# Kernel optimization log

Hardware: AMD Instinct MI355X
Metric: run time of the kernel (lower is better)

## Reference

```python
import jax, jax.numpy as jnp
import numpy as np

B = 2048; IN_DIM = 60; TTL = 30; H = 512; L = 5; OUT = 23
T_PTS = 90; SUB = 10  # fixed-step RK4 substeps per day (stands in for per-sample dopri5)
P_D = 0.2; P_H = 0.15; P_V = 0.25  # DELPHI fixed detection/hospitalization/ventilation fractions
LN2 = float(np.log(2.0))
R_I = LN2/5.0; R_D = LN2/2.0; R_RI = LN2/10.0; R_RH = LN2/15.0; R_RV = LN2/10.0


def setup_inputs():
    ks = jax.random.split(jax.random.key(0), 24)
    w = lambda k, s: (jax.random.normal(k, s) * 0.05).astype(jnp.float32)
    rng = jnp.array([1.0]*11 + [1.0, 60.0, 4.0, 0.5, 0.3, 0.5, 5.0, 5.0, 2.0, 60.0, 30.0, 1.0], dtype=jnp.float32)
    return {
        'model_input': jax.random.normal(ks[0], (B, IN_DIM), dtype=jnp.float32),
        'population': jax.random.uniform(ks[1], (B,), minval=1e5, maxval=1e7, dtype=jnp.float32),
        'cumulative_case_number': jax.random.uniform(ks[2], (B, 1), minval=1e3, maxval=1e5, dtype=jnp.float32),
        'mortality_rate': jax.random.uniform(ks[3], (B,), minval=0.01, maxval=0.05, dtype=jnp.float32),
        'h0': jax.random.normal(ks[4], (L, B, H), dtype=jnp.float32),
        'c0': jax.random.normal(ks[5], (L, B, H), dtype=jnp.float32),
        'W_ih0': w(ks[6], (4*H, TTL)),
        'W_ihR': w(ks[7], (L-1, 4*H, H)),
        'W_hh': w(ks[8], (L, 4*H, H)),
        'b_ih': w(ks[9], (L, 4*H)),
        'b_hh': w(ks[10], (L, 4*H)),
        'meta_W1': w(ks[11], (H, IN_DIM - TTL)), 'meta_b1': w(ks[12], (H,)),
        'meta_W2': w(ks[13], (H, H)), 'meta_b2': w(ks[14], (H,)),
        'ro_W1': w(ks[15], (2*H, 2*H)), 'ro_b1': w(ks[16], (2*H,)),
        'ro_W2': w(ks[17], (OUT, 2*H)), 'ro_b2': w(ks[18], (OUT,)),
        'dnn_output_range': rng,
        'sigmoid_scale': 1,
    }


def _backbone(model_input, population, h0, c0, W_ih0, W_ihR, W_hh, b_ih, b_hh,
              meta_W1, meta_b1, meta_W2, meta_b2, ro_W1, ro_b1, ro_W2, ro_b2,
              dnn_output_range, sigmoid_scale):
    x = model_input[:, :TTL] / population[:, None]
    for l in range(L):  # single-timestep, 5-layer LSTM; torch gate order i,f,g,o
        Wi = W_ih0 if l == 0 else W_ihR[l-1]
        g = x @ Wi.T + b_ih[l] + h0[l] @ W_hh[l].T + b_hh[l]
        gi, gf, gg, go = jnp.split(g, 4, axis=1)
        c = jax.nn.sigmoid(gf) * c0[l] + jax.nn.sigmoid(gi) * jnp.tanh(gg)
        x = jax.nn.sigmoid(go) * jnp.tanh(c)
    ts_out = x  # [B, H]
    m = jax.nn.relu(model_input[:, TTL:] @ meta_W1.T + meta_b1)
    m = jax.nn.relu(m @ meta_W2.T + meta_b2)
    z = jnp.concatenate([ts_out, m], axis=1)  # [B, 2H]
    z = jnp.tanh(z @ ro_W1.T + ro_b1)
    raw = z @ ro_W2.T + ro_b2  # [B, OUT]
    dnn = jax.nn.sigmoid(raw * sigmoid_scale) * dnn_output_range
    return dnn, ts_out, raw


def _ode(dnn, population, cumulative_case_number, mortality_rate):
    p = dnn[:, 11:]  # 12 fitted DELPHI params per sample
    alpha, days, r_s, r_dth, p_dth, r_dthdecay, k1, k2, jump, t_jump, std_normal, k3 = [p[:, j] for j in range(12)]
    N = population
    PopI = cumulative_case_number[:, 0]
    PopD = jnp.floor(mortality_rate * PopI)
    R_0 = jnp.where(PopI - PopD > 5.0 * PopD, 5.0 * PopD, 0.0)
    PopCI = PopI - PopD - R_0
    # DELPHI initial conditions
    S0 = N - (PopCI/P_D)*(k1 + k2) - R_0/P_D - PopD/P_D
    y0 = jnp.stack([
        S0,
        PopCI/P_D*k1,                      # E
        PopCI/P_D*k2,                      # I
        (PopCI/P_D - PopCI)*(1.0 - p_dth), # AR
        PopCI*P_H*(1.0 - p_dth),           # DHR
        PopCI*(1.0 - P_H)*(1.0 - p_dth),   # DQR
        (PopCI/P_D - PopCI)*p_dth,         # AD
        PopCI*P_H*p_dth,                   # DHD
        PopCI*(1.0 - P_H)*p_dth,           # DQD
        R_0/P_D,                           # R
        PopD/P_D,                          # D
        PopCI*P_H,                         # TH
        PopCI*P_H*P_V*(1.0 - p_dth),       # DVR
        PopCI*P_H*P_V*p_dth,               # DVD
        PopD,                              # DD
        PopI,                              # DT
    ], axis=1)  # [B, 16]

    def deriv(t, y):
        S, E, I = y[:, 0], y[:, 1], y[:, 2]
        AR, DHR, DQR, AD, DHD, DQD = y[:, 3], y[:, 4], y[:, 5], y[:, 6], y[:, 7], y[:, 8]
        DVR, DVD = y[:, 12], y[:, 13]
        gam = (2.0/jnp.pi)*jnp.arctan(-(t - days)/20.0*r_s) + 1.0 \
              + jump*jnp.exp(-(t - t_jump)**2/(2.0*std_normal**2))
        pdt = (2.0/jnp.pi)*(p_dth - 0.001)*(jnp.arctan(-t*r_dthdecay/20.0) + jnp.pi/2.0) + 0.001
        inf = alpha*gam*S*I/N
        det = R_D*I
        return jnp.stack([
            -inf,
            inf - R_I*E,
            R_I*E - det,
            det*(1.0-pdt)*(1.0-P_D) - R_RI*AR,
            det*(1.0-pdt)*P_D*P_H - R_RH*DHR,
            det*(1.0-pdt)*P_D*(1.0-P_H) - R_RI*DQR,
            det*pdt*(1.0-P_D) - r_dth*AD,
            det*pdt*P_D*P_H - r_dth*DHD,
            det*pdt*P_D*(1.0-P_H) - r_dth*DQD,
            R_RI*(AR + DQR) + R_RH*DHR,
            r_dth*(AD + DQD + DHD),
            det*P_D*P_H,
            det*(1.0-pdt)*P_D*P_H*P_V - R_RV*DVR,
            det*pdt*P_D*P_H*P_V - r_dth*DVD,
            r_dth*(DHD + DQD),
            det*P_D,
        ], axis=1)

    dt = 1.0 / SUB

    def segment(y, t0):
        def sub(yy, j):
            t = t0 + j*dt
            k1_ = deriv(t, yy)
            k2_ = deriv(t + 0.5*dt, yy + 0.5*dt*k1_)
            k3_ = deriv(t + 0.5*dt, yy + 0.5*dt*k2_)
            k4_ = deriv(t + dt, yy + dt*k3_)
            return yy + (dt/6.0)*(k1_ + 2.0*k2_ + 2.0*k3_ + k4_), None
        y2, _ = jax.lax.scan(sub, y, jnp.arange(SUB, dtype=jnp.float32))
        return y2, y2

    _, ys = jax.lax.scan(segment, y0, jnp.arange(T_PTS - 1, dtype=jnp.float32))
    sol = jnp.concatenate([y0[None], ys], axis=0)  # [T_PTS, B, 16]
    return jnp.transpose(sol, (1, 0, 2))  # [B, T_PTS, 16]


def reference(model_input, population, cumulative_case_number, mortality_rate, h0, c0,
              W_ih0, W_ihR, W_hh, b_ih, b_hh, meta_W1, meta_b1, meta_W2, meta_b2,
              ro_W1, ro_b1, ro_W2, ro_b2, dnn_output_range, sigmoid_scale):
    dnn, ts_out, raw = _backbone(model_input, population, h0, c0, W_ih0, W_ihR, W_hh,
                                 b_ih, b_hh, meta_W1, meta_b1, meta_W2, meta_b2,
                                 ro_W1, ro_b1, ro_W2, ro_b2, dnn_output_range, sigmoid_scale)
    sol = _ode(dnn, population, cumulative_case_number, mortality_rate)
    return sol, dnn, ts_out[:, None, :], raw
```

## Files before the change

kernel.cpp:

```cpp
#include <hip/hip_runtime.h>
#include <hip/hip_bf16.h>
#include <math.h>

#define BATCH 2048
#define HID 512
#define TPTS 90
#define NSEG 89
#define NSUB 10
#define NSTEPS 890

__device__ __constant__ const float kR_I  = 0.6931471805599453f / 5.0f;
__device__ __constant__ const float kR_D  = 0.6931471805599453f / 2.0f;
__device__ __constant__ const float kR_RI = 0.6931471805599453f / 10.0f;
__device__ __constant__ const float kR_RH = 0.6931471805599453f / 15.0f;
__device__ __constant__ const float kR_RV = 0.6931471805599453f / 10.0f;

typedef __attribute__((ext_vector_type(8))) short short8;
typedef __attribute__((ext_vector_type(4))) short short4v;
typedef __attribute__((ext_vector_type(4))) float float4v;

__device__ __forceinline__ float sigmoidf_(float x) { return 1.0f / (1.0f + expf(-x)); }

__global__ void prep_pad(const float* __restrict__ mi, const float* __restrict__ pop,
                         const float* __restrict__ Wih0, const float* __restrict__ mW1,
// ... 3 lines not shown
    int i = blockIdx.x * 256 + threadIdx.x;
    int r = i >> 5, c = i & 31;
    bool v = (c < 30);
    x0p[i] = v ? mi[r * 60 + c] / pop[r] : 0.0f;
    xmp[i] = v ? mi[r * 60 + 30 + c] : 0.0f;
    Wp0[i] = v ? Wih0[r * 30 + c] : 0.0f;
    if (r < 512) Wpm[i] = v ? mW1[r * 30 + c] : 0.0f;
}

__device__ __forceinline__ void pack_quad(const float* __restrict__ s1, int ld1, int K1,
                                          const float* __restrict__ s2, int ld2, int K2,
                                          __hip_bfloat16* __restrict__ dst, int idx, bool wm)
{
    int Ks = K1 + K2, Kq = Ks >> 2;
    int r = idx / Kq, k4 = (idx - r * Kq) << 2;
    const float* srcp; int base, seg, kk;
    if (k4 < K1) { srcp = s1 + (size_t)r * ld1 + k4; base = 0; seg = K1; kk = k4; }
    else { kk = k4 - K1; srcp = s2 + (size_t)r * ld2 + kk; base = 3 * K1; seg = K2; }
    float4 x = *(const float4*)srcp;
    union { __hip_bfloat16 b[4]; short4v v; } H, L;
    H.b[0] = __float2bfloat16(x.x); H.b[1] = __float2bfloat16(x.y);
    H.b[2] = __float2bfloat16(x.z); H.b[3] = __float2bfloat16(x.w);
    L.b[0] = __float2bfloat16(x.x - __bfloat162float(H.b[0]));
    L.b[1] = __float2bfloat16(x.y - __bfloat162float(H.b[1]));
    L.b[2] = __float2bfloat16(x.z - __bfloat162float(H.b[2]));
    L.b[3] = __float2bfloat16(x.w - __bfloat162float(H.b[3]));
    __hip_bfloat16* d = dst + (size_t)r * (3 * Ks) + base;
    *(short4v*)(d + kk)           = H.v;
    *(short4v*)(d + seg + kk)     = wm ? L.v : H.v;
    *(short4v*)(d + 2 * seg + kk) = wm ? H.v : L.v;
}

__global__ void pack_pair(const float* __restrict__ a1, int alda1, int aK1,
                          const float* __restrict__ a2, int alda2, int aK2,
                          __hip_bfloat16* __restrict__ da, int arows,
                          const float* __restrict__ w1, int wld1, int wK1,
                          const float* __restrict__ w2, int wld2, int wK2,
                          __hip_bfloat16* __restrict__ dw, int wrows)
{
    int aKq = (aK1 + aK2) >> 2, wKq = (wK1 + wK2) >> 2;
    int qa = arows * aKq;
    int idx = blockIdx.x * 256 + threadIdx.x;
    if (idx < qa) {
        pack_quad(a1, alda1, aK1, a2, alda2, aK2, da, idx, false);
    } else {
        idx -= qa;
        if (idx < wrows * wKq) pack_quad(w1, wld1, wK1, w2, wld2, wK2, dw, idx, true);
    }
}

template<int ACT>
__global__ __launch_bounds__(256, 2)
void gemm_mfma(const __hip_bfloat16* __restrict__ Ah,
               const __hip_bfloat16* __restrict__ Wh, int K3, int kHalf,
               const float* __restrict__ b1, const float* __restrict__ b2,
               float* __restrict__ Cp, float* __restrict__ Cp2, int ldc, int N)
{
    __shared__ __hip_bfloat16 As[128 * 32];
    __shared__ __hip_bfloat16 Ws[128 * 32];
    const int tid  = threadIdx.x;
    const int m0   = blockIdx.y * 128;
    const int n0   = blockIdx.x * 128;
    const int z    = blockIdx.z;
    const int k0   = z ? kHalf : 0;
    const int kLen = (kHalf == 0) ? K3 : (z ? (K3 - kHalf) : kHalf);
    float* C = z ? Cp2 : Cp;
    const int lane = tid & 63, wv = tid >> 6;
    const int mw   = (wv >> 1) * 64, nw = (wv & 1) * 64;
    const int l15  = lane & 15, quad = lane >> 4;
    const int sr   = tid >> 2;
    const int sc   = (tid & 3) * 8;

    float4v acc[4][4];
    #pragma unroll
    for (int i = 0; i < 4; ++i)
        #pragma unroll
        for (int j = 0; j < 4; ++j)
            acc[i][j] = (float4v){0.0f, 0.0f, 0.0f, 0.0f};

    const __hip_bfloat16* pa0 = Ah + (size_t)(m0 + sr)      * K3 + k0 + sc;
    const __hip_bfloat16* pa1 = Ah + (size_t)(m0 + sr + 64) * K3 + k0 + sc;
    const __hip_bfloat16* pw0 = Wh + (size_t)(n0 + sr)      * K3 + k0 + sc;
    const __hip_bfloat16* pw1 = Wh + (size_t)(n0 + sr + 64) * K3 + k0 + sc;

    short8 a0 = *(const short8*)(pa0);
    short8 a1 = *(const short8*)(pa1);
    short8 w0 = *(const short8*)(pw0);
    short8 w1 = *(const short8*)(pw1);

    for (int kt = 0; kt < kLen; kt += 32) {
        __syncthreads();
        *(short8*)(As + sr * 32 + sc)        = a0;
        *(short8*)(As + (sr + 64) * 32 + sc) = a1;
        *(short8*)(Ws + sr * 32 + sc)        = w0;
        *(short8*)(Ws + (sr + 64) * 32 + sc) = w1;
        __syncthreads();

        int kn = kt + 32;
        if (kn < kLen) {
            a0 = *(const short8*)(pa0 + kn);
            a1 = *(const short8*)(pa1 + kn);
            w0 = *(const short8*)(pw0 + kn);
            w1 = *(const short8*)(pw1 + kn);
        }

        short8 af[4], bf[4];
        #pragma unroll
        for (int t = 0; t < 4; ++t) {
            af[t] = *(const short8*)(As + (mw + t * 16 + l15) * 32 + quad * 8);
            bf[t] = *(const short8*)(Ws + (nw + t * 16 + l15) * 32 + quad * 8);
        }
        #pragma unroll
        for (int i = 0; i < 4; ++i)
            #pragma unroll
            for (int j = 0; j < 4; ++j)
                acc[i][j] = __builtin_amdgcn_mfma_f32_16x16x32_bf16(af[i], bf[j], acc[i][j], 0, 0, 0);
    }

    #pragma unroll
    for (int j = 0; j < 4; ++j) {
        int col = n0 + nw + j * 16 + l15;
        float bias = z ? 0.0f : (b1[col] + (b2 ? b2[col] : 0.0f));
        #pragma unroll
        for (int i = 0; i < 4; ++i) {
            #pragma unroll
            for (int r = 0; r < 4; ++r) {
                int row = m0 + mw + i * 16 + quad * 4 + r;
                float v = acc[i][j][r] + bias;
                if (ACT == 1)      v = fmaxf(v, 0.0f);
                else if (ACT == 2) v = tanhf(v);
                C[(size_t)row * ldc + col] = v;
            }
        }
    }
}

template<int ACT>
__global__ __launch_bounds__(256)
void gemm_dual(const float* __restrict__ A1, int lda1,
               const float* __restrict__ W1, int ldw1, int K1,
               const float* __restrict__ A2, int lda2,
               const float* __restrict__ W2, int ldw2, int K2,
               const float* __restrict__ b1p, const float* __restrict__ b2p,
               float* __restrict__ Cp, int ldc, int N)
{
    __shared__ float As[8][128];
    __shared__ float Ws[8][128];
    const int tid  = threadIdx.x;
    const int m0   = blockIdx.y * 128;
    const int n0   = blockIdx.x * 128;
    const int tm   = tid >> 4;
    const int tn   = tid & 15;
    const int lrow = tid >> 1;
    const int lkh  = (tid & 1) << 2;
    const int wrow = n0 + lrow;
    const int Ktot = K1 + K2;

    float acc[8][8];
    #pragma unroll
    for (int i = 0; i < 8; ++i)
        #pragma unroll
        for (int j = 0; j < 8; ++j) acc[i][j] = 0.0f;

    float4 av = *(const float4*)(A1 + (size_t)(m0 + lrow) * lda1 + lkh);
    float4 wv = make_float4(0.0f, 0.0f, 0.0f, 0.0f);
    if (wrow < N) wv = *(const float4*)(W1 + (size_t)wrow * ldw1 + lkh);

    for (int kt = 0; kt < Ktot; kt += 8) {
        __syncthreads();
        As[lkh + 0][lrow] = av.x; As[lkh + 1][lrow] = av.y;
        As[lkh + 2][lrow] = av.z; As[lkh + 3][lrow] = av.w;
        Ws[lkh + 0][lrow] = wv.x; Ws[lkh + 1][lrow] = wv.y;
        Ws[lkh + 2][lrow] = wv.z; Ws[lkh + 3][lrow] = wv.w;
        __syncthreads();

// ... 109 lines not shown
        const float* g2 = G1 + (size_t)m * 2048 + h;
        gi += g2[0]; gf += g2[512]; gg += g2[1024]; go += g2[1536];
    }
    float c = sigmoidf_(gf) * c0l[i] + sigmoidf_(gi) * tanhf(gg);
    float x = sigmoidf_(go) * tanhf(c);
    xout[(size_t)m * xld + h] = x;
    if (ts) ts[i] = x;
}

__global__ void dnn_kernel(const float* __restrict__ raw, const int* __restrict__ ssp,
                           const float* __restrict__ rng, float* __restrict__ dnn)
{
    int i = blockIdx.x * 256 + threadIdx.x;
    if (i >= 2048 * 23) return;
    int c = i % 23;
    int v = *ssp;
    float ss = (v > 100000 || v < 0) ? __int_as_float(v) : (float)v;
    dnn[i] = sigmoidf_(raw[i] * ss) * rng[c];
}

__device__ __forceinline__ void gampdt_eval(float t, float alpha, float days, float rs20,
                                            float jump, float t_jump, float inv2s2,
                                            float pconst, float rdd20, float* ag, float* pd)
{
    float dtj = t - t_jump;
    float g = 0.6366197723675814f * atanf((days - t) * rs20) + 1.0f + jump * expf(-(dtj * dtj) * inv2s2);
    *ag = alpha * g;
    *pd = pconst * (atanf(-t * rdd20) + 1.5707963267948966f) + 0.001f;
}

__global__ void gampdt4_kernel(const float* __restrict__ dnn, const float* __restrict__ pop,
                               float4* __restrict__ ag4)
{
    int idx = blockIdx.x * 256 + threadIdx.x;
    if (idx >= NSTEPS * 2048) return;
    int e = idx & 2047;
    int k = idx >> 11;
    int s = k / 10, j = k - s * 10;
    const float* p = dnn + e * 23 + 11;
    float alpha = p[0], days = p[1], r_s = p[2], p_dth = p[4], r_dthdecay = p[5];
    float jump = p[8], t_jump = p[9], stdn = p[10];
    float invN = 1.0f / pop[e];
    float rs20   = r_s * 0.05f;
    float rdd20  = r_dthdecay * 0.05f;
    float inv2s2 = 1.0f / (2.0f * stdn * stdn);
    float pconst = 0.6366197723675814f * (p_dth - 0.001f);
    float t = (float)s + (float)j * 0.1f;
    float agh, pdh, ag1, pd1;
    gampdt_eval(t + 0.05f, alpha, days, rs20, jump, t_jump, inv2s2, pconst, rdd20, &agh, &pdh);
    gampdt_eval(t + 0.1f,  alpha, days, rs20, jump, t_jump, inv2s2, pconst, rdd20, &ag1, &pd1);
    ag4[idx] = make_float4(agh * invN, pdh, ag1 * invN, pd1);
}

__global__ __launch_bounds__(64)
void ode_core(const float* __restrict__ dnn, const float* __restrict__ pop,
              const float* __restrict__ ccn, const float* __restrict__ mort,
              const float4* __restrict__ ag4, float4* __restrict__ det4,
              float* __restrict__ sol)
{
    int e = blockIdx.x * 64 + threadIdx.x;
    const float* p = dnn + e * 23 + 11;
    float alpha = p[0], days = p[1], r_s = p[2], k1p = p[6], k2p = p[7];
    float jump = p[8], t_jump = p[9], stdn = p[10], p_dth = p[4], rdd = p[5];

    float N = pop[e];
    float invN = 1.0f / N;
    float PopI = ccn[e];
    float PopD = floorf(mort[e] * PopI);
    float R0v  = (PopI - PopD > 5.0f * PopD) ? 5.0f * PopD : 0.0f;
    float PopCI = PopI - PopD - R0v;
    float DP = PopCI / 0.2f;

    float y0 = N - DP * (k1p + k2p) - R0v / 0.2f - PopD / 0.2f;
    float y1 = DP * k1p;
    float y2 = DP * k2p;
    float y11 = PopCI * 0.15f;
    float y15 = PopI;

    float* sole = sol + (size_t)e * (TPTS * 16);
    sole[0] = y0; sole[1] = y1; sole[2] = y2; sole[11] = y11; sole[15] = y15;

    float rs20   = r_s * 0.05f;
    float rdd20  = rdd * 0.05f;
    float inv2s2 = 1.0f / (2.0f * stdn * stdn);
    float pconst = 0.6366197723675814f * (p_dth - 0.001f);
    float ag0, pd0;
    gampdt_eval(0.0f, alpha, days, rs20, jump, t_jump, inv2s2, pconst, rdd20, &ag0, &pd0);
    float agI = ag0 * invN;

    float4 cv[10];
    #pragma unroll
    for (int j = 0; j < 10; ++j) cv[j] = ag4[(size_t)j * 2048 + e];

    const float h6 = 0.016666668f;
    for (int s = 0; s < NSEG; ++s) {
        float Sdet = 0.0f;
        float4 db[10];
        #pragma unroll
        for (int j = 0; j < 10; ++j) {
            float agh = cv[j].x, ag1 = cv[j].z;
            int kn = (s + 1) * 10 + j;
            if (kn >= NSTEPS) kn = NSTEPS - 1;
            cv[j] = ag4[(size_t)kn * 2048 + e];

            float det1 = kR_D * y2;
            float t1   = kR_I * y1;
            float inf  = agI * y0 * y2;
            float d1 = inf - t1, d2 = t1 - det1;
            float a0 = -inf, a1 = d1, a2 = d2;
            float z0 = y0 - 0.05f * inf, z1 = y1 + 0.05f * d1, z2 = y2 + 0.05f * d2;
            float det2 = kR_D * z2; t1 = kR_I * z1; inf = agh * z0 * z2;
            d1 = inf - t1; d2 = t1 - det2;
            a0 -= 2.0f * inf; a1 += 2.0f * d1; a2 += 2.0f * d2;
            z0 = y0 - 0.05f * inf; z1 = y1 + 0.05f * d1; z2 = y2 + 0.05f * d2;
            float det3 = kR_D * z2; t1 = kR_I * z1; inf = agh * z0 * z2;
            d1 = inf - t1; d2 = t1 - det3;
            a0 -= 2.0f * inf; a1 += 2.0f * d1; a2 += 2.0f * d2;
            z0 = y0 - 0.1f * inf; z1 = y1 + 0.1f * d1; z2 = y2 + 0.1f * d2;
            float det4v = kR_D * z2; t1 = kR_I * z1; inf = ag1 * z0 * z2;
            d1 = inf - t1; d2 = t1 - det4v;
            a0 -= inf; a1 += d1; a2 += d2;

            y0 += h6 * a0; y1 += h6 * a1; y2 += h6 * a2;
            float Wd = det1;
            Wd += 2.0f * det2; Wd += 2.0f * det3; Wd += det4v;
            Sdet += Wd;
            db[j] = make_float4(det1, det2, det3, det4v);
            agI = ag1;
        }
        #pragma unroll
        for (int j = 0; j < 10; ++j)
            det4[(size_t)(s * 10 + j) * 2048 + e] = db[j];
        y11 += h6 * (0.03f * Sdet);
        y15 += h6 * (0.2f * Sdet);
        float* sp = sole + (size_t)(s + 1) * 16;
        sp[0] = y0; sp[1] = y1; sp[2] = y2; sp[11] = y11; sp[15] = y15;
    }
}

__global__ __launch_bounds__(64)
void ode_decay(const float* __restrict__ dnn, const float* __restrict__ ccn,
               const float* __restrict__ mort, const float4* __restrict__ ag4,
               const float4* __restrict__ det4, float* __restrict__ sol)
{
    const int t  = blockIdx.x * 64 + threadIdx.x;
    const int e  = t >> 3;
    const int g  = t & 7;
    const int lane = threadIdx.x & 63;
    const int base = lane & ~7;

    const float* p = dnn + e * 23 + 11;
    float r_dth = p[3], p_dth = p[4];

    float PopI = ccn[e];
    float PopD = floorf(mort[e] * PopI);
    float R0v  = (PopI - PopD > 5.0f * PopD) ? 5.0f * PopD : 0.0f;
    float PopCI = PopI - PopD - R0v;
    float DP = PopCI / 0.2f;
    float ompd = 1.0f - p_dth;

    float iy3  = (DP - PopCI) * ompd;
    float iy4  = PopCI * 0.15f * ompd;
    float iy5  = PopCI * 0.85f * ompd;
    float iy6  = (DP - PopCI) * p_dth;
    float iy7  = PopCI * 0.15f * p_dth;
    float iy8  = PopCI * 0.85f * p_dth;
    float iy12 = PopCI * 0.15f * 0.25f * ompd;
    float iy13 = PopCI * 0.15f * 0.25f * p_dth;

    float ha = (g == 0) ? iy3 : (g == 1) ? iy4 : (g == 2) ? iy5 : iy6;
    float hb = (g == 4) ? iy7 : (g == 5) ? iy8 : (g == 6) ? iy12 : iy13;
    float ys = (g < 4) ? ha : hb;
    float c1 = (g == 0) ? 0.8f : (g == 1) ? 0.03f : (g == 2) ? 0.17f : (g == 6) ? 0.0075f : 0.0f;
    float c2 = (g == 3) ? 0.8f : (g == 4) ? 0.03f : (g == 5) ? 0.17f : (g == 7) ? 0.0075f : 0.0f;
    float rr = (g == 0 || g == 2) ? kR_RI : (g == 1) ? kR_RH : (g == 6) ? kR_RV : r_dth;
    int own_idx = (g < 4) ? ((g < 2) ? (g == 0 ? 3 : 4) : (g == 2 ? 5 : 6))
                          : ((g < 6) ? (g == 4 ? 7 : 8) : (g == 6 ? 12 : 13));

    float y9  = R0v / 0.2f;
    float y10 = PopD / 0.2f;
    float y14 = PopD;

    float* sole = sol + (size_t)e * (TPTS * 16);
    sole[own_idx] = ys;
    if (g == 0) sole[9]  = y9;
    if (g == 1) sole[10] = y10;
    if (g == 2) sole[14] = y14;

    float pconst = 0.6366197723675814f * (p_dth - 0.001f);
    float pd0 = pconst * 1.5707963267948966f + 0.001f;
    float u0 = c1 * (1.0f - pd0) + c2 * pd0;

    float4 cvd[10], cva[10];
    #pragma unroll
    for (int j = 0; j < 10; ++j) {
        cvd[j] = det4[(size_t)j * 2048 + e];
        cva[j] = ag4[(size_t)j * 2048 + e];
    }

    const float h6 = 0.016666668f;
    for (int s = 0; s < NSEG; ++s) {
        float Sy = 0.0f;
        #pragma unroll
        for (int j = 0; j < 10; ++j) {
            float4 dd = cvd[j];
            float pdh = cva[j].y, pd1 = cva[j].w;
            int kn = (s + 1) * 10 + j;
            if (kn >= NSTEPS) kn = NSTEPS - 1;
            cvd[j] = det4[(size_t)kn * 2048 + e];
            cva[j] = ag4[(size_t)kn * 2048 + e];

            float uh = c1 * (1.0f - pdh) + c2 * pdh;
            float u1 = c1 * (1.0f - pd1) + c2 * pd1;
            float k1v = dd.x * u0 - rr * ys;
            float zs1 = ys + 0.05f * k1v;
            float k2v = dd.y * uh - rr * zs1;
            float zs2 = ys + 0.05f * k2v;
            float k3v = dd.z * uh - rr * zs2;
            float zs3 = ys + 0.1f * k3v;
            float k4v = dd.w * u1 - rr * zs3;
            float ka = k1v + 2.0f * (k2v + k3v) + k4v;
            Sy += ys + 2.0f * (zs1 + zs2) + zs3;
            ys += h6 * ka;
            u0 = u1;
        }
        float S0 = __shfl(Sy, base + 0, 64);
        float S1 = __shfl(Sy, base + 1, 64);
        float S2 = __shfl(Sy, base + 2, 64);
        float S3 = __shfl(Sy, base + 3, 64);
        float S4 = __shfl(Sy, base + 4, 64);
        float S5 = __shfl(Sy, base + 5, 64);
        y9  += h6 * (kR_RI * (S0 + S2) + kR_RH * S1);
        y10 += h6 * (r_dth * ((S3 + S4) + S5));
        y14 += h6 * (r_dth * (S4 + S5));

        float* sp = sole + (size_t)(s + 1) * 16;
        sp[own_idx] = ys;
        if (g == 0) sp[9]  = y9;
        if (g == 1) sp[10] = y10;
        if (g == 2) sp[14] = y14;
    }
}

__device__ __forceinline__ void deriv16(const float* y, float ag, float pd,
                                        float invN, float r_dth, float* d)
{
    float inf = ag * y[0] * y[2] * invN;
    float det = kR_D * y[2];
    float t1  = kR_I * y[1];
    float omp = 1.0f - pd;
    float dq  = det * omp;
    float dp  = det * pd;
    float dq003 = dq * 0.03f;
    float dp003 = dp * 0.03f;
    d[0]  = -inf;
    d[1]  = inf - t1;
    d[2]  = t1 - det;
    d[3]  = dq * 0.8f  - kR_RI * y[3];
    d[4]  = dq003      - kR_RH * y[4];
    d[5]  = dq * 0.17f - kR_RI * y[5];
    d[6]  = dp * 0.8f  - r_dth * y[6];
    d[7]  = dp003      - r_dth * y[7];
    d[8]  = dp * 0.17f - r_dth * y[8];
    d[9]  = kR_RI * (y[3] + y[5]) + kR_RH * y[4];
    d[10] = r_dth * ((y[6] + y[7]) + y[8]);
    d[11] = det * 0.03f;
    d[12] = 0.25f * dq003 - kR_RV * y[12];
    d[13] = 0.25f * dp003 - r_dth * y[13];
    d[14] = r_dth * (y[7] + y[8]);
    d[15] = det * 0.2f;
}

__global__ __launch_bounds__(64)
void ode_kernel(const float* __restrict__ dnn, const float* __restrict__ pop,
                const float* __restrict__ ccn, const float* __restrict__ mort,
                float* __restrict__ sol)
{
    int e = blockIdx.x * 64 + threadIdx.x;
    const float* p = dnn + e * 23 + 11;
    float alpha = p[0], days = p[1], r_s = p[2], r_dth = p[3], p_dth = p[4];
    float r_dthdecay = p[5], k1p = p[6], k2p = p[7], jump = p[8], t_jump = p[9], stdn = p[10];

    float N = pop[e];
    float invN = 1.0f / N;
    float PopI = ccn[e];
    float PopD = floorf(mort[e] * PopI);
    float R0v  = (PopI - PopD > 5.0f * PopD) ? 5.0f * PopD : 0.0f;
    float PopCI = PopI - PopD - R0v;
    float DP = PopCI / 0.2f;

    float y[16];
    y[0]  = N - DP * (k1p + k2p) - R0v / 0.2f - PopD / 0.2f;
    y[1]  = DP * k1p;
    y[2]  = DP * k2p;
    y[3]  = (DP - PopCI) * (1.0f - p_dth);
    y[4]  = PopCI * 0.15f * (1.0f - p_dth);
    y[5]  = PopCI * 0.85f * (1.0f - p_dth);
    y[6]  = (DP - PopCI) * p_dth;
    y[7]  = PopCI * 0.15f * p_dth;
    y[8]  = PopCI * 0.85f * p_dth;
    y[9]  = R0v / 0.2f;
    y[10] = PopD / 0.2f;
    y[11] = PopCI * 0.15f;
    y[12] = PopCI * 0.15f * 0.25f * (1.0f - p_dth);
    y[13] = PopCI * 0.15f * 0.25f * p_dth;
    y[14] = PopD;
    y[15] = PopI;

    {
        float* sp = sol + (size_t)e * (TPTS * 16);
        #pragma unroll
        for (int i = 0; i < 16; ++i) sp[i] = y[i];
    }

    float rs20   = r_s * 0.05f;
    float rdd20  = r_dthdecay * 0.05f;
    float inv2s2 = 1.0f / (2.0f * stdn * stdn);
    float pconst = 0.6366197723675814f * (p_dth - 0.001f);

    float ag0, pd0;
    gampdt_eval(0.0f, alpha, days, rs20, jump, t_jump, inv2s2, pconst, rdd20, &ag0, &pd0);

    for (int s = 0; s < NSEG; ++s) {
        float t0 = (float)s;
        for (int j = 0; j < NSUB; ++j) {
            float agh, pdh, ag1, pd1;
// ... 15 lines not shown
            for (int i = 0; i < 16; ++i) y[i] += 0.016666668f * (acc[i] + d[i]);
            ag0 = ag1; pd0 = pd1;
        }
        float* sp = sol + (size_t)e * (TPTS * 16) + (size_t)(s + 1) * 16;
        #pragma unroll
        for (int i = 0; i < 16; ++i) sp[i] = y[i];
    }
}

extern "C" void kernel_launch(void* const* d_in, const int* in_sizes, int n_in,
                              void* d_out, int out_size, void* d_ws, size_t ws_size,
                              hipStream_t stream)
{
    const float* mi   = (const float*)d_in[0];
    const float* pop  = (const float*)d_in[1];
    const float* ccn  = (const float*)d_in[2];
    const float* mort = (const float*)d_in[3];
    const float* h0   = (const float*)d_in[4];
    const float* c0   = (const float*)d_in[5];
    const float* Wih0 = (const float*)d_in[6];
    const float* WihR = (const float*)d_in[7];
    const float* Whh  = (const float*)d_in[8];
    const float* bih  = (const float*)d_in[9];
    const float* bhh  = (const float*)d_in[10];
    const float* mW1  = (const float*)d_in[11];
    const float* mb1  = (const float*)d_in[12];
    const float* mW2  = (const float*)d_in[13];
    const float* mb2  = (const float*)d_in[14];
    const float* rW1  = (const float*)d_in[15];
    const float* rb1  = (const float*)d_in[16];
    const float* rW2  = (const float*)d_in[17];
    const float* rb2  = (const float*)d_in[18];
    const float* rng  = (const float*)d_in[19];
    const int*   ssp  = (const int*)d_in[20];

    float* out   = (float*)d_out;
    float* sol_o = out;
    float* dnn_o = out + 2949120;
    float* ts_o  = out + 2949120 + 47104;
    float* raw_o = out + 2949120 + 47104 + 1048576;

    float* ws  = (float*)d_ws;
    float* G   = ws;
    float* Z   = ws + 4194304;
    float* X0  = ws + 6291456;
    float* X1  = ws + 7340032;
    float* x0p = ws + 8388608;
    float* xmp = ws + 8454144;
    float* Wp0 = ws + 8519680;
    float* Wpm = ws + 8585216;
    __hip_bfloat16* Ab = (__hip_bfloat16*)(ws + 8601600);
    __hip_bfloat16* Wb = (__hip_bfloat16*)(ws + 8601600 + 3145728);
    float4* AG4  = (float4*)(ws + 8601600);
    float4* DET4 = (float4*)ws;
    float*  G1   = ws + 15892480;
    bool wsOK  = ws_size >= (size_t)15892480 * sizeof(float);
    bool wsOK2 = ws_size >= (size_t)(15892480 + 4194304) * sizeof(float);

    prep_pad<<<256, 256, 0, stream>>>(mi, pop, Wih0, mW1, x0p, xmp, Wp0, Wpm);

    gemm_dual<1><<<dim3(4, 16), 256, 0, stream>>>(xmp, 32, Wpm, 32, 32,
                                                  nullptr, 0, nullptr, 0, 0,
                                                  mb1, nullptr, G, 512, 512);

    if (wsOK) {
        pack_pair<<<(2048 * 128 + 512 * 128 + 255) / 256, 256, 0, stream>>>(
            G, 512, 512, nullptr, 0, 0, Ab, 2048,
            mW2, 512, 512, nullptr, 0, 0, Wb, 512);
        gemm_mfma<1><<<dim3(4, 16, 1), 256, 0, stream>>>(Ab, Wb, 1536, 0, mb2, nullptr,
                                                         Z + 512, nullptr, 1024, 512);

        for (int l = 0; l < 5; ++l) {
            const float* A1 = (l == 0) ? x0p : ((l & 1) ? X1 : X0);
            int          K1 = (l == 0) ? 32 : 512;
            const float* W1 = (l == 0) ? Wp0 : (WihR + (size_t)(l - 1) * 1048576);
            int Ks = K1 + 512, K3 = 3 * Ks, Kq = Ks >> 2;
            pack_pair<<<(2048 * Kq * 2 + 255) / 256, 256, 0, stream>>>(
                A1, K1, K1, h0 + (size_t)l * 1048576, 512, 512, Ab, 2048,
                W1, K1, K1, Whh + (size_t)l * 1048576, 512, 512, Wb, 2048);
            int kh = wsOK2 ? (((K3 / 2) + 31) / 32) * 32 : 0;
            gemm_mfma<0><<<dim3(16, 16, wsOK2 ? 2 : 1), 256, 0, stream>>>(
                Ab, Wb, K3, kh, bih + l * 2048, bhh + l * 2048, G, G1, 2048, 2048);
            float* xo  = (l == 4) ? Z : ((l & 1) ? X0 : X1);
            int    xol = (l == 4) ? 1024 : 512;
            lstm_gates<<<4096, 256, 0, stream>>>(G, wsOK2 ? G1 : nullptr,
                                                 c0 + (size_t)l * 1048576, xo, xol,
                                                 (l == 4) ? ts_o : nullptr);
        }

        pack_pair<<<(2048 * 256 + 1024 * 256 + 255) / 256, 256, 0, stream>>>(
            Z, 1024, 1024, nullptr, 0, 0, Ab, 2048,
            rW1, 1024, 1024, nullptr, 0, 0, Wb, 1024);
        if (wsOK2) {
            gemm_mfma<0><<<dim3(8, 16, 2), 256, 0, stream>>>(Ab, Wb, 3072, 1536, rb1, nullptr,
                                                             G, G1, 1024, 1024);
            gemv_ro2<<<512, 256, 0, stream>>>(G, G1, rW2, rb2, ssp, rng, raw_o, dnn_o);
        } else {
            gemm_mfma<2><<<dim3(8, 16, 1), 256, 0, stream>>>(Ab, Wb, 3072, 0, rb1, nullptr,
                                                             G, nullptr, 1024, 1024);
            gemv_ro2<<<512, 256, 0, stream>>>(G, nullptr, rW2, rb2, ssp, rng, raw_o, dnn_o);
        }

        gampdt4_kernel<<<(NSTEPS * 2048 + 255) / 256, 256, 0, stream>>>(dnn_o, pop, AG4);
        ode_core<<<32, 64, 0, stream>>>(dnn_o, pop, ccn, mort, AG4, DET4, sol_o);
        ode_decay<<<256, 64, 0, stream>>>(dnn_o, ccn, mort, AG4, DET4, sol_o);
    } else {
        gemm_dual<1><<<dim3(4, 16), 256, 0, stream>>>(G, 512, mW2, 512, 512,
                                                      nullptr, 0, nullptr, 0, 0,
                                                      mb2, nullptr, Z + 512, 1024, 512);
        for (int l = 0; l < 5; ++l) {
            const float* A1 = (l == 0) ? x0p : ((l & 1) ? X1 : X0);
            int          K1 = (l == 0) ? 32 : 512;
            const float* W1 = (l == 0) ? Wp0 : (WihR + (size_t)(l - 1) * 1048576);
            gemm_dual<0><<<dim3(16, 16), 256, 0, stream>>>(
                A1, K1, W1, K1, K1,
                h0 + (size_t)l * 1048576, 512, Whh + (size_t)l * 1048576, 512, 512,
                bih + l * 2048, bhh + l * 2048, G, 2048, 2048);
            float* xo  = (l == 4) ? Z : ((l & 1) ? X0 : X1);
            int    xol = (l == 4) ? 1024 : 512;
            lstm_gates<<<4096, 256, 0, stream>>>(G, nullptr, c0 + (size_t)l * 1048576, xo, xol,
                                                 (l == 4) ? ts_o : nullptr);
        }
        gemm_dual<2><<<dim3(8, 16), 256, 0, stream>>>(Z, 1024, rW1, 1024, 1024,
                                                      nullptr, 0, nullptr, 0, 0,
                                                      rb1, nullptr, G, 1024, 1024);
        gemm_dual<0><<<dim3(1, 16), 256, 0, stream>>>(G, 1024, rW2, 1024, 1024,
                                                      nullptr, 0, nullptr, 0, 0,
                                                      rb2, nullptr, raw_o, 23, 23);
        dnn_kernel<<<184, 256, 0, stream>>>(raw_o, ssp, rng, dnn_o);
        ode_kernel<<<32, 64, 0, stream>>>(dnn_o, pop, ccn, mort, sol_o);
    }
    (void)in_sizes; (void)n_in; (void)out_size;
}
```

Measured before the change: 724.1 us.

## Fuse ODE core and decay kernels into one producer-consumer block kernel

Merges the two sequential ODE kernels into one kernel per 64 samples. One wavefront integrates the S/E/I core state and writes detection terms into a double-buffered shared-memory ring, while eight consumer wavefronts integrate the decay compartments one segment behind. This removes the global DET4 round trip and the second launch, and lets the two serial chains overlap. The cost is a block-wide barrier every segment, and only 32 blocks on the device. The GEMM split-K is also generalised to N chunks, though it still uses two.

```diff
diff --git a/kernel.cpp b/kernel.cpp
--- a/kernel.cpp
+++ b/kernel.cpp
@@ -79,9 +79,10 @@
 template<int ACT>
 __global__ __launch_bounds__(256, 2)
 void gemm_mfma(const __hip_bfloat16* __restrict__ Ah,
-               const __hip_bfloat16* __restrict__ Wh, int K3, int kHalf,
+               const __hip_bfloat16* __restrict__ Wh, int K3, int kChunk,
                const float* __restrict__ b1, const float* __restrict__ b2,
-               float* __restrict__ Cp, float* __restrict__ Cp2, int ldc, int N)
+               float* __restrict__ Cp, float* __restrict__ Cp2,
+               int ldc, int N)
 {
     __shared__ __hip_bfloat16 As[128 * 32];
     __shared__ __hip_bfloat16 Ws[128 * 32];
@@ -89,9 +90,10 @@
     const int m0   = blockIdx.y * 128;
     const int n0   = blockIdx.x * 128;
     const int z    = blockIdx.z;
-    const int k0   = z ? kHalf : 0;
-    const int kLen = (kHalf == 0) ? K3 : (z ? (K3 - kHalf) : kHalf);
-    float* C = z ? Cp2 : Cp;
+    const int k0   = z * kChunk;
+    int kLen = (kChunk == 0) ? K3 : (K3 - k0 < kChunk ? K3 - k0 : kChunk);
+    if (kLen < 0) kLen = 0;
+    float* C = (z == 0) ? Cp : Cp2;
     const int lane = tid & 63, wv = tid >> 6;
     const int mw   = (wv >> 1) * 64, nw = (wv & 1) * 64;
     const int l15  = lane & 15, quad = lane >> 4;
@@ -110,10 +112,13 @@
     const __hip_bfloat16* pw0 = Wh + (size_t)(n0 + sr)      * K3 + k0 + sc;
     const __hip_bfloat16* pw1 = Wh + (size_t)(n0 + sr + 64) * K3 + k0 + sc;
 
-    short8 a0 = *(const short8*)(pa0);
-    short8 a1 = *(const short8*)(pa1);
-    short8 w0 = *(const short8*)(pw0);
-    short8 w1 = *(const short8*)(pw1);
+    short8 a0 = {0,0,0,0,0,0,0,0}, a1 = a0, w0 = a0, w1 = a0;
+    if (kLen > 0) {
+        a0 = *(const short8*)(pa0);
+        a1 = *(const short8*)(pa1);
+        w0 = *(const short8*)(pw0);
+        w1 = *(const short8*)(pw1);
+    }
 
     for (int kt = 0; kt < kLen; kt += 32) {
         __syncthreads();
@@ -147,7 +152,7 @@
     #pragma unroll
     for (int j = 0; j < 4; ++j) {
         int col = n0 + nw + j * 16 + l15;
-        float bias = z ? 0.0f : (b1[col] + (b2 ? b2[col] : 0.0f));
+        float bias = (z == 0) ? (b1[col] + (b2 ? b2[col] : 0.0f)) : 0.0f;
         #pragma unroll
         for (int i = 0; i < 4; ++i) {
             #pragma unroll
@@ -363,193 +368,191 @@
     ag4[idx] = make_float4(agh * invN, pdh, ag1 * invN, pd1);
 }
 
-__global__ __launch_bounds__(64)
-void ode_core(const float* __restrict__ dnn, const float* __restrict__ pop,
-              const float* __restrict__ ccn, const float* __restrict__ mort,
-              const float4* __restrict__ ag4, float4* __restrict__ det4,
-              float* __restrict__ sol)
-{
-    int e = blockIdx.x * 64 + threadIdx.x;
-    const float* p = dnn + e * 23 + 11;
-    float alpha = p[0], days = p[1], r_s = p[2], k1p = p[6], k2p = p[7];
-    float jump = p[8], t_jump = p[9], stdn = p[10], p_dth = p[4], rdd = p[5];
-
-    float N = pop[e];
-    float invN = 1.0f / N;
-    float PopI = ccn[e];
-    float PopD = floorf(mort[e] * PopI);
-    float R0v  = (PopI - PopD > 5.0f * PopD) ? 5.0f * PopD : 0.0f;
-    float PopCI = PopI - PopD - R0v;
-    float DP = PopCI / 0.2f;
-
-    float y0 = N - DP * (k1p + k2p) - R0v / 0.2f - PopD / 0.2f;
-    float y1 = DP * k1p;
-    float y2 = DP * k2p;
-    float y11 = PopCI * 0.15f;
-    float y15 = PopI;
-
-    float* sole = sol + (size_t)e * (TPTS * 16);
-    sole[0] = y0; sole[1] = y1; sole[2] = y2; sole[11] = y11; sole[15] = y15;
-
-    float rs20   = r_s * 0.05f;
-    float rdd20  = rdd * 0.05f;
-    float inv2s2 = 1.0f / (2.0f * stdn * stdn);
-    float pconst = 0.6366197723675814f * (p_dth - 0.001f);
-    float ag0, pd0;
-    gampdt_eval(0.0f, alpha, days, rs20, jump, t_jump, inv2s2, pconst, rdd20, &ag0, &pd0);
-    float agI = ag0 * invN;
-
-    float4 cv[10];
-    #pragma unroll
-    for (int j = 0; j < 10; ++j) cv[j] = ag4[(size_t)j * 2048 + e];
-
+__global__ __launch_bounds__(576, 1)
+void ode_fused(const float* __restrict__ dnn, const float* __restrict__ pop,
+               const float* __restrict__ ccn, const float* __restrict__ mort,
+               const float4* __restrict__ ag4, float* __restrict__ sol)
+{
+    __shared__ float4 sdet[2][10][64];
+    const int tid  = threadIdx.x;
+    const int wvid = tid >> 6;
+    const int lane = tid & 63;
     const float h6 = 0.016666668f;
-    for (int s = 0; s < NSEG; ++s) {
-        float Sdet = 0.0f;
-        float4 db[10];
-        #pragma unroll
-        for (int j = 0; j < 10; ++j) {
-            float agh = cv[j].x, ag1 = cv[j].z;
-            int kn = (s + 1) * 10 + j;
-            if (kn >= NSTEPS) kn = NSTEPS - 1;
-            cv[j] = ag4[(size_t)kn * 2048 + e];
-
-            float det1 = kR_D * y2;
-            float t1   = kR_I * y1;
-            float inf  = agI * y0 * y2;
-            float d1 = inf - t1, d2 = t1 - det1;
-            float a0 = -inf, a1 = d1, a2 = d2;
-            float z0 = y0 - 0.05f * inf, z1 = y1 + 0.05f * d1, z2 = y2 + 0.05f * d2;
-            float det2 = kR_D * z2; t1 = kR_I * z1; inf = agh * z0 * z2;
-            d1 = inf - t1; d2 = t1 - det2;
-            a0 -= 2.0f * inf; a1 += 2.0f * d1; a2 += 2.0f * d2;
-            z0 = y0 - 0.05f * inf; z1 = y1 + 0.05f * d1; z2 = y2 + 0.05f * d2;
-            float det3 = kR_D * z2; t1 = kR_I * z1; inf = agh * z0 * z2;
-            d1 = inf - t1; d2 = t1 - det3;
-            a0 -= 2.0f * inf; a1 += 2.0f * d1; a2 += 2.0f * d2;
-            z0 = y0 - 0.1f * inf; z1 = y1 + 0.1f * d1; z2 = y2 + 0.1f * d2;
-            float det4v = kR_D * z2; t1 = kR_I * z1; inf = ag1 * z0 * z2;
-            d1 = inf - t1; d2 = t1 - det4v;
-            a0 -= inf; a1 += d1; a2 += d2;
-
-            y0 += h6 * a0; y1 += h6 * a1; y2 += h6 * a2;
-            float Wd = det1;
-            Wd += 2.0f * det2; Wd += 2.0f * det3; Wd += det4v;
-            Sdet += Wd;
-            db[j] = make_float4(det1, det2, det3, det4v);
-            agI = ag1;
-        }
-        #pragma unroll
-        for (int j = 0; j < 10; ++j)
-            det4[(size_t)(s * 10 + j) * 2048 + e] = db[j];
-        y11 += h6 * (0.03f * Sdet);
-        y15 += h6 * (0.2f * Sdet);
-        float* sp = sole + (size_t)(s + 1) * 16;
-        sp[0] = y0; sp[1] = y1; sp[2] = y2; sp[11] = y11; sp[15] = y15;
-    }
-}
-
-__global__ __launch_bounds__(64)
-void ode_decay(const float* __restrict__ dnn, const float* __restrict__ ccn,
-               const float* __restrict__ mort, const float4* __restrict__ ag4,
-               const float4* __restrict__ det4, float* __restrict__ sol)
-{
-    const int t  = blockIdx.x * 64 + threadIdx.x;
-    const int e  = t >> 3;
-    const int g  = t & 7;
-    const int lane = threadIdx.x & 63;
-    const int base = lane & ~7;
-
-    const float* p = dnn + e * 23 + 11;
-    float r_dth = p[3], p_dth = p[4];
-
-    float PopI = ccn[e];
-    float PopD = floorf(mort[e] * PopI);
-    float R0v  = (PopI - PopD > 5.0f * PopD) ? 5.0f * PopD : 0.0f;
-    float PopCI = PopI - PopD - R0v;
-    float DP = PopCI / 0.2f;
-    float ompd = 1.0f - p_dth;
-
-    float iy3  = (DP - PopCI) * ompd;
-    float iy4  = PopCI * 0.15f * ompd;
-    float iy5  = PopCI * 0.85f * ompd;
-    float iy6  = (DP - PopCI) * p_dth;
-    float iy7  = PopCI * 0.15f * p_dth;
-    float iy8  = PopCI * 0.85f * p_dth;
-    float iy12 = PopCI * 0.15f * 0.25f * ompd;
-    float iy13 = PopCI * 0.15f * 0.25f * p_dth;
-
-    float ha = (g == 0) ? iy3 : (g == 1) ? iy4 : (g == 2) ? iy5 : iy6;
-    float hb = (g == 4) ? iy7 : (g == 5) ? iy8 : (g == 6) ? iy12 : iy13;
-    float ys = (g < 4) ? ha : hb;
-    float c1 = (g == 0) ? 0.8f : (g == 1) ? 0.03f : (g == 2) ? 0.17f : (g == 6) ? 0.0075f : 0.0f;
-    float c2 = (g == 3) ? 0.8f : (g == 4) ? 0.03f : (g == 5) ? 0.17f : (g == 7) ? 0.0075f : 0.0f;
-    float rr = (g == 0 || g == 2) ? kR_RI : (g == 1) ? kR_RH : (g == 6) ? kR_RV : r_dth;
-    int own_idx = (g < 4) ? ((g < 2) ? (g == 0 ? 3 : 4) : (g == 2 ? 5 : 6))
-                          : ((g < 6) ? (g == 4 ? 7 : 8) : (g == 6 ? 12 : 13));
-
-    float y9  = R0v / 0.2f;
-    float y10 = PopD / 0.2f;
-    float y14 = PopD;
-
-    float* sole = sol + (size_t)e * (TPTS * 16);
-    sole[own_idx] = ys;
-    if (g == 0) sole[9]  = y9;
-    if (g == 1) sole[10] = y10;
-    if (g == 2) sole[14] = y14;
-
-    float pconst = 0.6366197723675814f * (p_dth - 0.001f);
-    float pd0 = pconst * 1.5707963267948966f + 0.001f;
-    float u0 = c1 * (1.0f - pd0) + c2 * pd0;
-
-    float4 cvd[10], cva[10];
-    #pragma unroll
-    for (int j = 0; j < 10; ++j) {
-        cvd[j] = det4[(size_t)j * 2048 + e];
-        cva[j] = ag4[(size_t)j * 2048 + e];
-    }
-
-    const float h6 = 0.016666668f;
-    for (int s = 0; s < NSEG; ++s) {
-        float Sy = 0.0f;
-        #pragma unroll
-        for (int j = 0; j < 10; ++j) {
-            float4 dd = cvd[j];
-            float pdh = cva[j].y, pd1 = cva[j].w;
-            int kn = (s + 1) * 10 + j;
-            if (kn >= NSTEPS) kn = NSTEPS - 1;
-            cvd[j] = det4[(size_t)kn * 2048 + e];
-            cva[j] = ag4[(size_t)kn * 2048 + e];
-
-            float uh = c1 * (1.0f - pdh) + c2 * pdh;
-            float u1 = c1 * (1.0f - pd1) + c2 * pd1;
-            float k1v = dd.x * u0 - rr * ys;
-            float zs1 = ys + 0.05f * k1v;
-            float k2v = dd.y * uh - rr * zs1;
-            float zs2 = ys + 0.05f * k2v;
-            float k3v = dd.z * uh - rr * zs2;
-            float zs3 = ys + 0.1f * k3v;
-            float k4v = dd.w * u1 - rr * zs3;
-            float ka = k1v + 2.0f * (k2v + k3v) + k4v;
-            Sy += ys + 2.0f * (zs1 + zs2) + zs3;
-            ys += h6 * ka;
-            u0 = u1;
-        }
-        float S0 = __shfl(Sy, base + 0, 64);
-        float S1 = __shfl(Sy, base + 1, 64);
-        float S2 = __shfl(Sy, base + 2, 64);
-        float S3 = __shfl(Sy, base + 3, 64);
-        float S4 = __shfl(Sy, base + 4, 64);
-        float S5 = __shfl(Sy, base + 5, 64);
-        y9  += h6 * (kR_RI * (S0 + S2) + kR_RH * S1);
-        y10 += h6 * (r_dth * ((S3 + S4) + S5));
-        y14 += h6 * (r_dth * (S4 + S5));
-
-        float* sp = sole + (size_t)(s + 1) * 16;
-        sp[own_idx] = ys;
-        if (g == 0) sp[9]  = y9;
-        if (g == 1) sp[10] = y10;
-        if (g == 2) sp[14] = y14;
+
+    if (wvid == 0) {
+        int e = blockIdx.x * 64 + lane;
+        const float* p = dnn + e * 23 + 11;
+        float alpha = p[0], days = p[1], r_s = p[2], k1p = p[6], k2p = p[7];
+        float jump = p[8], t_jump = p[9], stdn = p[10], p_dth = p[4], rdd = p[5];
+
+        float N = pop[e];
+        float invN = 1.0f / N;
+        float PopI = ccn[e];
+        float PopD = floorf(mort[e] * PopI);
+        float R0v  = (PopI - PopD > 5.0f * PopD) ? 5.0f * PopD : 0.0f;
+        float PopCI = PopI - PopD - R0v;
+        float DP = PopCI / 0.2f;
+
+        float y0 = N - DP * (k1p + k2p) - R0v / 0.2f - PopD / 0.2f;
+        float y1 = DP * k1p;
+        float y2 = DP * k2p;
+        float y11 = PopCI * 0.15f;
+        float y15 = PopI;
+
+        float* sole = sol + (size_t)e * (TPTS * 16);
+        sole[0] = y0; sole[1] = y1; sole[2] = y2; sole[11] = y11; sole[15] = y15;
+
+        float rs20   = r_s * 0.05f;
+        float rdd20  = rdd * 0.05f;
+        float inv2s2 = 1.0f / (2.0f * stdn * stdn);
+        float pconst = 0.6366197723675814f * (p_dth - 0.001f);
+        float ag0, pd0;
+        gampdt_eval(0.0f, alpha, days, rs20, jump, t_jump, inv2s2, pconst, rdd20, &ag0, &pd0);
+        float agI = ag0 * invN;
+
+        float4 cv[10];
+        #pragma unroll
+        for (int j = 0; j < 10; ++j) cv[j] = ag4[(size_t)j * 2048 + e];
+
+        for (int s = 0; s <= NSEG; ++s) {
+            if (s < NSEG) {
+                float Sdet = 0.0f;
+                #pragma unroll
+                for (int j = 0; j < 10; ++j) {
+                    float agh = cv[j].x, ag1 = cv[j].z;
+                    int kn = (s + 1) * 10 + j;
+                    if (kn >= NSTEPS) kn = NSTEPS - 1;
+                    cv[j] = ag4[(size_t)kn * 2048 + e];
+
+                    float det1 = kR_D * y2;
+                    float t1   = kR_I * y1;
+                    float inf  = agI * y0 * y2;
+                    float d1 = inf - t1, d2 = t1 - det1;
+                    float a0 = -inf, a1 = d1, a2 = d2;
+                    float z0 = y0 - 0.05f * inf, z1 = y1 + 0.05f * d1, z2 = y2 + 0.05f * d2;
+                    float det2 = kR_D * z2; t1 = kR_I * z1; inf = agh * z0 * z2;
+                    d1 = inf - t1; d2 = t1 - det2;
+                    a0 -= 2.0f * inf; a1 += 2.0f * d1; a2 += 2.0f * d2;
+                    z0 = y0 - 0.05f * inf; z1 = y1 + 0.05f * d1; z2 = y2 + 0.05f * d2;
+                    float det3 = kR_D * z2; t1 = kR_I * z1; inf = agh * z0 * z2;
+                    d1 = inf - t1; d2 = t1 - det3;
+                    a0 -= 2.0f * inf; a1 += 2.0f * d1; a2 += 2.0f * d2;
+                    z0 = y0 - 0.1f * inf; z1 = y1 + 0.1f * d1; z2 = y2 + 0.1f * d2;
+                    float det4v = kR_D * z2; t1 = kR_I * z1; inf = ag1 * z0 * z2;
+                    d1 = inf - t1; d2 = t1 - det4v;
+                    a0 -= inf; a1 += d1; a2 += d2;
+
+                    y0 += h6 * a0; y1 += h6 * a1; y2 += h6 * a2;
+                    float Wd = det1;
+                    Wd += 2.0f * det2; Wd += 2.0f * det3; Wd += det4v;
+                    Sdet += Wd;
+                    sdet[s & 1][j][lane] = make_float4(det1, det2, det3, det4v);
+                    agI = ag1;
+                }
+                y11 += h6 * (0.03f * Sdet);
+                y15 += h6 * (0.2f * Sdet);
+                float* sp = sole + (size_t)(s + 1) * 16;
+                sp[0] = y0; sp[1] = y1; sp[2] = y2; sp[11] = y11; sp[15] = y15;
+            }
+            __syncthreads();
+        }
+    } else {
+        const int dl = tid - 64;
+        const int cl = dl >> 3;
+        const int g  = dl & 7;
+        const int base = lane & ~7;
+        int e = blockIdx.x * 64 + cl;
+
+        const float* p = dnn + e * 23 + 11;
+        float r_dth = p[3], p_dth = p[4];
+
+        float PopI = ccn[e];
+        float PopD = floorf(mort[e] * PopI);
+        float R0v  = (PopI - PopD > 5.0f * PopD) ? 5.0f * PopD : 0.0f;
+        float PopCI = PopI - PopD - R0v;
+        float DP = PopCI / 0.2f;
+        float ompd = 1.0f - p_dth;
+
+        float iy3  = (DP - PopCI) * ompd;
+        float iy4  = PopCI * 0.15f * ompd;
+        float iy5  = PopCI * 0.85f * ompd;
+        float iy6  = (DP - PopCI) * p_dth;
+        float iy7  = PopCI * 0.15f * p_dth;
+        float iy8  = PopCI * 0.85f * p_dth;
+        float iy12 = PopCI * 0.15f * 0.25f * ompd;
+        float iy13 = PopCI * 0.15f * 0.25f * p_dth;
+
+        float ha = (g == 0) ? iy3 : (g == 1) ? iy4 : (g == 2) ? iy5 : iy6;
+        float hb = (g == 4) ? iy7 : (g == 5) ? iy8 : (g == 6) ? iy12 : iy13;
+        float ys = (g < 4) ? ha : hb;
+        float c1 = (g == 0) ? 0.8f : (g == 1) ? 0.03f : (g == 2) ? 0.17f : (g == 6) ? 0.0075f : 0.0f;
+        float c2 = (g == 3) ? 0.8f : (g == 4) ? 0.03f : (g == 5) ? 0.17f : (g == 7) ? 0.0075f : 0.0f;
+        float rr = (g == 0 || g == 2) ? kR_RI : (g == 1) ? kR_RH : (g == 6) ? kR_RV : r_dth;
+        int own_idx = (g < 4) ? ((g < 2) ? (g == 0 ? 3 : 4) : (g == 2 ? 5 : 6))
+                              : ((g < 6) ? (g == 4 ? 7 : 8) : (g == 6 ? 12 : 13));
+
+        float y9  = R0v / 0.2f;
+        float y10 = PopD / 0.2f;
+        float y14 = PopD;
+
+        float* sole = sol + (size_t)e * (TPTS * 16);
+        sole[own_idx] = ys;
+        if (g == 0) sole[9]  = y9;
+        if (g == 1) sole[10] = y10;
+        if (g == 2) sole[14] = y14;
+
+        float pconst = 0.6366197723675814f * (p_dth - 0.001f);
+        float pd0 = pconst * 1.5707963267948966f + 0.001f;
+        float u0 = c1 * (1.0f - pd0) + c2 * pd0;
+
+        float4 cva[10];
+        #pragma unroll
+        for (int j = 0; j < 10; ++j) cva[j] = ag4[(size_t)j * 2048 + e];
+
+        for (int s = 0; s <= NSEG; ++s) {
+            if (s > 0) {
+                const int sp_ = s - 1;
+                float Sy = 0.0f;
+                #pragma unroll
+                for (int j = 0; j < 10; ++j) {
+                    float4 dd = sdet[sp_ & 1][j][cl];
+                    float pdh = cva[j].y, pd1 = cva[j].w;
+                    int kn = (sp_ + 1) * 10 + j;
+                    if (kn >= NSTEPS) kn = NSTEPS - 1;
+                    cva[j] = ag4[(size_t)kn * 2048 + e];
+
+                    float uh = c1 * (1.0f - pdh) + c2 * pdh;
+                    float u1 = c1 * (1.0f - pd1) + c2 * pd1;
+                    float k1v = dd.x * u0 - rr * ys;
+                    float zs1 = ys + 0.05f * k1v;
+                    float k2v = dd.y * uh - rr * zs1;
+                    float zs2 = ys + 0.05f * k2v;
+                    float k3v = dd.z * uh - rr * zs2;
+                    float zs3 = ys + 0.1f * k3v;
+                    float k4v = dd.w * u1 - rr * zs3;
+                    float ka = k1v + 2.0f * (k2v + k3v) + k4v;
+                    Sy += ys + 2.0f * (zs1 + zs2) + zs3;
+                    ys += h6 * ka;
+                    u0 = u1;
+                }
+                float S0 = __shfl(Sy, base + 0, 64);
+                float S1 = __shfl(Sy, base + 1, 64);
+                float S2 = __shfl(Sy, base + 2, 64);
+                float S3 = __shfl(Sy, base + 3, 64);
+                float S4 = __shfl(Sy, base + 4, 64);
+                float S5 = __shfl(Sy, base + 5, 64);
+                y9  += h6 * (kR_RI * (S0 + S2) + kR_RH * S1);
+                y10 += h6 * (r_dth * ((S3 + S4) + S5));
+                y14 += h6 * (r_dth * (S4 + S5));
+
+                float* spp = sole + (size_t)sp_ * 16 + 16;
+                spp[own_idx] = ys;
+                if (g == 0) spp[9]  = y9;
+                if (g == 1) spp[10] = y10;
+                if (g == 2) spp[14] = y14;
+            }
+            __syncthreads();
+        }
     }
 }
 
@@ -582,7 +585,7 @@
     d[15] = det * 0.2f;
 }
 
-__global__ __launch_bounds__(64)
+__global__ __launch_bounds__(64, 1)
 void ode_kernel(const float* __restrict__ dnn, const float* __restrict__ pop,
                 const float* __restrict__ ccn, const float* __restrict__ mort,
                 float* __restrict__ sol)
@@ -704,10 +707,10 @@
     __hip_bfloat16* Ab = (__hip_bfloat16*)(ws + 8601600);
     __hip_bfloat16* Wb = (__hip_bfloat16*)(ws + 8601600 + 3145728);
     float4* AG4  = (float4*)(ws + 8601600);
-    float4* DET4 = (float4*)ws;
     float*  G1   = ws + 15892480;
     bool wsOK  = ws_size >= (size_t)15892480 * sizeof(float);
     bool wsOK2 = ws_size >= (size_t)(15892480 + 4194304) * sizeof(float);
+    int  nspl  = wsOK2 ? 2 : 1;
 
     prep_pad<<<256, 256, 0, stream>>>(mi, pop, Wih0, mW1, x0p, xmp, Wp0, Wpm);
 
@@ -716,6 +719,8 @@
                                                   mb1, nullptr, G, 512, 512);
 
     if (wsOK) {
+        float* g1p = (nspl >= 2) ? G1 : nullptr;
+
         pack_pair<<<(2048 * 128 + 512 * 128 + 255) / 256, 256, 0, stream>>>(
             G, 512, 512, nullptr, 0, 0, Ab, 2048,
             mW2, 512, 512, nullptr, 0, 0, Wb, 512);
@@ -730,12 +735,12 @@
             pack_pair<<<(2048 * Kq * 2 + 255) / 256, 256, 0, stream>>>(
                 A1, K1, K1, h0 + (size_t)l * 1048576, 512, 512, Ab, 2048,
                 W1, K1, K1, Whh + (size_t)l * 1048576, 512, 512, Wb, 2048);
-            int kh = wsOK2 ? (((K3 / 2) + 31) / 32) * 32 : 0;
-            gemm_mfma<0><<<dim3(16, 16, wsOK2 ? 2 : 1), 256, 0, stream>>>(
-                Ab, Wb, K3, kh, bih + l * 2048, bhh + l * 2048, G, G1, 2048, 2048);
+            int kc = (nspl > 1) ? (((K3 / nspl) + 31) / 32) * 32 : 0;
+            gemm_mfma<0><<<dim3(16, 16, nspl), 256, 0, stream>>>(
+                Ab, Wb, K3, kc, bih + l * 2048, bhh + l * 2048, G, G1, 2048, 2048);
             float* xo  = (l == 4) ? Z : ((l & 1) ? X0 : X1);
             int    xol = (l == 4) ? 1024 : 512;
-            lstm_gates<<<4096, 256, 0, stream>>>(G, wsOK2 ? G1 : nullptr,
+            lstm_gates<<<4096, 256, 0, stream>>>(G, g1p,
                                                  c0 + (size_t)l * 1048576, xo, xol,
                                                  (l == 4) ? ts_o : nullptr);
         }
@@ -743,10 +748,11 @@
         pack_pair<<<(2048 * 256 + 1024 * 256 + 255) / 256, 256, 0, stream>>>(
             Z, 1024, 1024, nullptr, 0, 0, Ab, 2048,
             rW1, 1024, 1024, nullptr, 0, 0, Wb, 1024);
-        if (wsOK2) {
-            gemm_mfma<0><<<dim3(8, 16, 2), 256, 0, stream>>>(Ab, Wb, 3072, 1536, rb1, nullptr,
-                                                             G, G1, 1024, 1024);
-            gemv_ro2<<<512, 256, 0, stream>>>(G, G1, rW2, rb2, ssp, rng, raw_o, dnn_o);
+        if (nspl > 1) {
+            int kc = (((3072 / nspl) + 31) / 32) * 32;
+            gemm_mfma<0><<<dim3(8, 16, nspl), 256, 0, stream>>>(Ab, Wb, 3072, kc, rb1, nullptr,
+                                                                G, G1, 1024, 1024);
+            gemv_ro2<<<512, 256, 0, stream>>>(G, g1p, rW2, rb2, ssp, rng, raw_o, dnn_o);
         } else {
             gemm_mfma<2><<<dim3(8, 16, 1), 256, 0, stream>>>(Ab, Wb, 3072, 0, rb1, nullptr,
                                                              G, nullptr, 1024, 1024);
@@ -754,8 +760,7 @@
         }
 
         gampdt4_kernel<<<(NSTEPS * 2048 + 255) / 256, 256, 0, stream>>>(dnn_o, pop, AG4);
-        ode_core<<<32, 64, 0, stream>>>(dnn_o, pop, ccn, mort, AG4, DET4, sol_o);
-        ode_decay<<<256, 64, 0, stream>>>(dnn_o, ccn, mort, AG4, DET4, sol_o);
+        ode_fused<<<32, 576, 0, stream>>>(dnn_o, pop, ccn, mort, AG4, sol_o);
     } else {
         gemm_dual<1><<<dim3(4, 16), 256, 0, stream>>>(G, 512, mW2, 512, 512,
                                                       nullptr, 0, nullptr, 0, 0,
@@ -770,7 +775,8 @@
                 bih + l * 2048, bhh + l * 2048, G, 2048, 2048);
             float* xo  = (l == 4) ? Z : ((l & 1) ? X0 : X1);
             int    xol = (l == 4) ? 1024 : 512;
-            lstm_gates<<<4096, 256, 0, stream>>>(G, nullptr, c0 + (size_t)l * 1048576, xo, xol,
+            lstm_gates<<<4096, 256, 0, stream>>>(G, nullptr,
+                                                 c0 + (size_t)l * 1048576, xo, xol,
                                                  (l == 4) ? ts_o : nullptr);
         }
         gemm_dual<2><<<dim3(8, 16), 256, 0, stream>>>(Z, 1024, rW1, 1024, 1024,
```

New measurement: 738.6 us. About the same (+2.0%).
